# Kernel tuning notes

Measured on AMD Instinct MI355X. Metric: run time of the kernel, lower is better.

The kernel has to match this reference:

```python
import jax, jax.numpy as jnp
import numpy as np


def _gru_step(h, x, Wih, Whh, bih, bhh):
    # PyTorch GRU cell: gates ordered (r, z, n)
    gi = x @ Wih.T + bih
    gh = h @ Whh.T + bhh
    ir, iz, inn = jnp.split(gi, 3, axis=-1)
    hr, hz, hn = jnp.split(gh, 3, axis=-1)
    r = jax.nn.sigmoid(ir + hr)
    u = jax.nn.sigmoid(iz + hz)
    n = jnp.tanh(inn + r * hn)
    return (1.0 - u) * n + u * h


def _forward(mini_batch, eps, W_ih1, W_hh1, b_ih1, b_hh1, W_ih2, W_hh2, b_ih2, b_hh2,
             h1_0, h2_0, Wt1, bt1, Wloc, bloc, Wsc, bsc, We1, be1, We2, be2, We3, be3):
    B = mini_batch.shape[0]
    x_tbf = jnp.swapaxes(mini_batch, 0, 1)      # [T,B,dim_x]
    eps_tbf = jnp.swapaxes(eps, 0, 1)           # [T,B,dim_z]
    h2_init = jnp.broadcast_to(h2_0, (B, h2_0.shape[0]))
    h1_init = jnp.broadcast_to(h1_0, (B, h1_0.shape[0]))

    # gen_RNN_2 over full sequence (all seq_lengths == T, pack/pad is identity)
    def scan2(h, x):
        h = _gru_step(h, x, W_ih2, W_hh2, b_ih2, b_hh2)
        return h, h
    _, h2_seq = jax.lax.scan(scan2, h2_init, x_tbf)              # [T,B,dim_h2]
    # at step t the emitter sees h2_output[t-2] (h2_0 for t==1): shift right by one
    h2_shift = jnp.concatenate([h2_init[None], h2_seq[:-1]], axis=0)

    def step(h1, inp):
        eps_t, h2_t = inp
        # stoch_trans (dz): MLP -> z_loc, z_scale
        hid = jax.nn.relu(h1 @ Wt1.T + bt1)
        z_loc = hid @ Wloc.T + bloc
        z_scale = jax.nn.softplus(hid @ Wsc.T + bsc)
        z_t = z_loc + z_scale * eps_t                            # reparameterized sample
        h1n = _gru_step(h1, z_t, W_ih1, W_hh1, b_ih1, b_hh1)     # gen_RNN_1 one step
        dx_in = jnp.concatenate([h1n, h2_t], axis=-1)            # [B, dim_h1+dim_h2]
        e = jax.nn.relu(dx_in @ We1.T + be1)                     # emitter (dx)
        e = jax.nn.relu(e @ We2.T + be2)
        x_ps = jax.nn.sigmoid(e @ We3.T + be3)                   # Bernoulli probs
        return h1n, x_ps

    _, xps = jax.lax.scan(step, h1_init, (eps_tbf, h2_shift))    # [T,B,dim_x]
    return jnp.swapaxes(xps, 0, 1)                               # [B,T,dim_x]


def setup_inputs() -> dict:
    key = jax.random.key(0)
    B, T = 256, 1000
    DX, DZ, H1, H2, DDX, DDZ = 100, 100, 10, 10, 20, 20
    ks = jax.random.split(key, 24)
    f32 = jnp.float32
    w = lambda k, shape: (jax.random.normal(k, shape, f32) * 0.1)
    inp = {
        "mini_batch": (jax.random.uniform(ks[0], (B, T, DX)) < 0.5).astype(f32),
        "eps": jax.random.normal(ks[1], (B, T, DZ), f32),
        # gen_RNN_1: input dim_z -> hidden dim_h1
        "W_ih1": w(ks[2], (3 * H1, DZ)), "W_hh1": w(ks[3], (3 * H1, H1)),
        "b_ih1": w(ks[4], (3 * H1,)), "b_hh1": w(ks[5], (3 * H1,)),
        # gen_RNN_2: input dim_x -> hidden dim_h2
        "W_ih2": w(ks[6], (3 * H2, DX)), "W_hh2": w(ks[7], (3 * H2, H2)),
        "b_ih2": w(ks[8], (3 * H2,)), "b_hh2": w(ks[9], (3 * H2,)),
        "h1_0": jnp.zeros((H1,), f32), "h2_0": jnp.zeros((H2,), f32),
        # stoch_trans (dz): dim_h1 -> dim_dz -> (dim_z loc, dim_z scale)
        "Wt1": w(ks[10], (DDZ, H1)), "bt1": w(ks[11], (DDZ,)),
        "Wloc": w(ks[12], (DZ, DDZ)), "bloc": w(ks[13], (DZ,)),
        "Wsc": w(ks[14], (DZ, DDZ)), "bsc": w(ks[15], (DZ,)),
        # emitter (dx): (dim_h1+dim_h2) -> dim_dx -> dim_dx -> dim_x, sigmoid
        "We1": w(ks[16], (DDX, H1 + H2)), "be1": w(ks[17], (DDX,)),
        "We2": w(ks[18], (DDX, DDX)), "be2": w(ks[19], (DDX,)),
        "We3": w(ks[20], (DX, DDX)), "be3": w(ks[21], (DX,)),
    }
    return inp


def reference(mini_batch, eps, W_ih1, W_hh1, b_ih1, b_hh1, W_ih2, W_hh2, b_ih2, b_hh2,
              h1_0, h2_0, Wt1, bt1, Wloc, bloc, Wsc, bsc, We1, be1, We2, be2, We3, be3):
    return _forward(mini_batch, eps, W_ih1, W_hh1, b_ih1, b_hh1, W_ih2, W_hh2, b_ih2, b_hh2,
                    h1_0, h2_0, Wt1, bt1, Wloc, bloc, Wsc, bsc, We1, be1, We2, be2, We3, be3)
```

## Files before the change

### kernel.cpp

```cpp
#include <hip/hip_runtime.h>
#include <cstdint>

#define T_LEN 1000
#define NB    256

typedef float v2f __attribute__((ext_vector_type(2)));

__device__ __forceinline__ float rcpf_(float x)     { return __builtin_amdgcn_rcpf(x); }
__device__ __forceinline__ float sigmoidf_(float x) { return rcpf_(1.f + __expf(-x)); }
__device__ __forceinline__ float tanhf_(float x) {
    float e = __expf(2.f * x);
    return 1.f - 2.f * rcpf_(e + 1.f);
}
__device__ __forceinline__ float softplusf_(float x) {
    return fmaxf(x, 0.f) + __logf(1.f + __expf(-fabsf(x)));
}
__device__ __forceinline__ float bcast_(float v, int l) {
    return __uint_as_float(__builtin_amdgcn_readlane(__float_as_uint(v), l));
}
__device__ __forceinline__ v2f pkfma_(v2f a, v2f b, v2f c) {
    v2f d;
    asm("v_pk_fma_f32 %0, %1, %2, %3" : "=v"(d) : "v"(a), "v"(b), "v"(c));
    return d;
}

__global__ __launch_bounds__(256) void gi2_kernel(
    const float* __restrict__ x, const float* __restrict__ W,
    const float* __restrict__ bias, float* __restrict__ out)
{
    __shared__ float xsT[100 * 67];

    const int tid = threadIdx.x;
    const int64_t base = (int64_t)blockIdx.x * (64 * 100);
    const float4* gx = (const float4*)(x + base);

#pragma unroll
    for (int it = 0; it < 7; ++it) {
        int i = tid + it * 256;
        if (i < 1600) {
            int r  = i / 25;
            int k4 = i - r * 25;
            float4 v = gx[i];
            xsT[(4 * k4 + 0) * 67 + r] = v.x;
            xsT[(4 * k4 + 1) * 67 + r] = v.y;
            xsT[(4 * k4 + 2) * 67 + r] = v.z;
            xsT[(4 * k4 + 3) * 67 + r] = v.w;
        }
    }
    __syncthreads();

    const int lane = tid & 63;
    const int wv   = __builtin_amdgcn_readfirstlane(tid >> 6);
    const int j0   = wv * 8;

    float acc[8];
#pragma unroll
    for (int jj = 0; jj < 8; ++jj) acc[jj] = 0.f;

    for (int k = 0; k < 100; ++k) {
        float xv = xsT[k * 67 + lane];
#pragma unroll
        for (int jj = 0; jj < 8; ++jj) {
            int j = j0 + jj; j = j > 29 ? 29 : j;
            acc[jj] = fmaf(xv, W[j * 100 + k], acc[jj]);
        }
    }
    float* orow = out + base + (int64_t)lane * 100;
#pragma unroll
    for (int jj = 0; jj < 8; ++jj) {
        int j = j0 + jj;
        if (j < 30) orow[j] = acc[jj] + bias[j];
    }
}

__global__ __launch_bounds__(128) void scan_kernel(
    const float* __restrict__ eps,
    const float* __restrict__ W_ih1, const float* __restrict__ W_hh1,
    const float* __restrict__ b_ih1, const float* __restrict__ b_hh1,
    const float* __restrict__ W_hh2, const float* __restrict__ b_hh2,
    const float* __restrict__ h1_0,  const float* __restrict__ h2_0,
    const float* __restrict__ Wt1,   const float* __restrict__ bt1,
    const float* __restrict__ Wloc,  const float* __restrict__ bloc,
    const float* __restrict__ Wsc,   const float* __restrict__ bsc,
    const float* __restrict__ We1,   const float* __restrict__ be1,
    const float* __restrict__ We2,   const float* __restrict__ be2,
    const float* __restrict__ We3,   const float* __restrict__ be3,
    float* out)
{
    __shared__ __align__(16) float ss[104];
    __shared__ __align__(16) float sh1ring[2][12];

    const int lane = threadIdx.x & 63;
    const int64_t rowbase = (int64_t)blockIdx.x * T_LEN * 100;
    const int wave = __builtin_amdgcn_readfirstlane((int)(threadIdx.x >> 6));

    if (wave == 0) {
        const int j   = lane & 31;
        const int jc  = j < 30 ? j : 29;
        const int h   = lane >> 5;
        const int lt  = lane < 20 ? lane : 19;
        const int k50 = lane < 50 ? lane : 49;

        float wt1r[10], whh1r[10], Cr[20];
        v2f wsc2[20], wbig2[26];
#pragma unroll
        for (int k = 0; k < 10; ++k) {
            wt1r[k]  = Wt1[lt * 10 + k];
            whh1r[k] = W_hh1[jc * 10 + k];
        }
        float bt1r  = bt1[lt];
        float bhh1r = b_hh1[jc];
        float br1   = b_ih1[jc];
#pragma unroll
        for (int l = 0; l < 20; ++l) {
            wsc2[l].x = Wsc[(2 * k50)     * 20 + l];
            wsc2[l].y = Wsc[(2 * k50 + 1) * 20 + l];
        }
        float bscx = bsc[2 * k50], bscy = bsc[2 * k50 + 1];
#pragma unroll
        for (int c = 0; c < 13; ++c) {
#pragma unroll
            for (int d = 0; d < 2; ++d) {
                int i0 = 4 * c + 2 * d;
                v2f w; w.x = 0.f; w.y = 0.f;
                if (i0     < 50) w.x = W_ih1[jc * 100 + 50 * h + i0];
                if (i0 + 1 < 50) w.y = W_ih1[jc * 100 + 50 * h + i0 + 1];
                wbig2[2 * c + d] = w;
            }
        }

        float dr = 0.f;
#pragma unroll
        for (int l = 0; l < 20; ++l) Cr[l] = 0.f;
        for (int kk = 0; kk < 100; ++kk) {
            float w = W_ih1[jc * 100 + kk];
            dr = fmaf(w, bloc[kk], dr);
#pragma unroll
            for (int l = 0; l < 20; ++l) Cr[l] = fmaf(w, Wloc[kk * 20 + l], Cr[l]);
        }

        if (lane < 2) { ss[50 + lane] = 0.f; ss[102 + lane] = 0.f; }

        float h1keep = h1_0[lane < 10 ? lane : 0];
        float sh1_[10];
#pragma unroll
        for (int k = 0; k < 10; ++k) sh1_[k] = h1_0[k];

        const float* erow = eps + rowbase;
        const int sidx = 2 * k50 + (k50 >= 25 ? 2 : 0);
        v2f ecur = *(const v2f*)(erow + 2 * k50);
        v2f enxt = *(const v2f*)(erow + 100 + 2 * k50);

#pragma unroll 1
        for (int t = 0; t <= T_LEN; ++t) {
            if (t < T_LEN) {
                v2f efut; efut.x = 0.f; efut.y = 0.f;
                if (t + 2 < T_LEN)
                    efut = *(const v2f*)(erow + (int64_t)(t + 2) * 100 + 2 * k50);

                float ha = bt1r, hb = 0.f, ga = bhh1r, gb = 0.f;
#pragma unroll
                for (int k = 0; k < 5; ++k) {
                    ha = fmaf(wt1r[2 * k],      sh1_[2 * k],     ha);
                    hb = fmaf(wt1r[2 * k + 1],  sh1_[2 * k + 1], hb);
                    ga = fmaf(whh1r[2 * k],     sh1_[2 * k],     ga);
                    gb = fmaf(whh1r[2 * k + 1], sh1_[2 * k + 1], gb);
                }
                float hidv = fmaxf(ha + hb, 0.f);
                float gh1v = ga + gb;

                float sgh[20];
#pragma unroll
                for (int l = 0; l < 20; ++l) sgh[l] = bcast_(hidv, l);

                float sA0 = bscx, sA1 = 0.f, sB0 = bscy, sB1 = 0.f, q0 = dr, q1 = 0.f;
#pragma unroll
                for (int l = 0; l < 10; ++l) {
                    sA0 = fmaf(wsc2[2 * l].x,     sgh[2 * l],     sA0);
                    sA1 = fmaf(wsc2[2 * l + 1].x, sgh[2 * l + 1], sA1);
                    sB0 = fmaf(wsc2[2 * l].y,     sgh[2 * l],     sB0);
                    sB1 = fmaf(wsc2[2 * l + 1].y, sgh[2 * l + 1], sB1);
                    q0  = fmaf(Cr[2 * l],         sgh[2 * l],     q0);
                    q1  = fmaf(Cr[2 * l + 1],     sgh[2 * l + 1], q1);
                }
                float gq = q0 + q1;
                float zx = softplusf_(sA0 + sA1) * ecur.x;
                float zy = softplusf_(sB0 + sB1) * ecur.y;
                if (lane < 50) {
                    v2f zp; zp.x = zx; zp.y = zy;
                    *(v2f*)(&ss[sidx]) = zp;
                }
                ecur = enxt; enxt = efut;
                __builtin_amdgcn_wave_barrier();

                const float4* sp4 = (const float4*)(&ss[52 * h]);
                v2f a0; a0.x = 0.f; a0.y = 0.f;
                v2f a1 = a0;
#pragma unroll
                for (int c = 0; c < 13; ++c) {
                    float4 v = sp4[c];
                    v2f vlo; vlo.x = v.x; vlo.y = v.y;
                    v2f vhi; vhi.x = v.z; vhi.y = v.w;
                    a0 = pkfma_(wbig2[2 * c],     vlo, a0);
                    a1 = pkfma_(wbig2[2 * c + 1], vhi, a1);
                }
                float p = (a0.x + a0.y) + (a1.x + a1.y);
                float gi1v = p + __shfl_xor(p, 32) + br1 + gq;
                float av   = gi1v + gh1v;
                float a10  = __shfl(av,   lane + 10);
                float gin  = __shfl(gi1v, lane + 20);
                float ghn  = __shfl(gh1v, lane + 20);
                if (lane < 10) {
                    float r = sigmoidf_(av);
                    float u = sigmoidf_(a10);
                    float n = tanhf_(fmaf(r, ghn, gin));
                    h1keep = fmaf(u, h1keep - n, n);
                    sh1ring[t & 1][lane] = h1keep;
                }
#pragma unroll
                for (int k = 0; k < 10; ++k) sh1_[k] = bcast_(h1keep, k);
            }
            __syncthreads();
        }
    } else {
        const int lt20 = lane < 20 ? lane : 19;
        const int l30  = lane < 30 ? lane : 29;
        const int ls   = lane < 50 ? lane : 49;

        float whh2r[10];
#pragma unroll
        for (int k = 0; k < 10; ++k) whh2r[k] = W_hh2[l30 * 10 + k];
        float bhh2r = b_hh2[l30];

        float we1r[20], we2r[20], we3A[20], we3B[20];
#pragma unroll
        for (int k = 0; k < 20; ++k) {
            we1r[k] = We1[lt20 * 20 + k];
            we2r[k] = We2[lt20 * 20 + k];
            we3A[k] = We3[ls * 20 + k];
            we3B[k] = We3[(ls + 50) * 20 + k];
        }
        float be1r = be1[lt20], be2r = be2[lt20];
        float be3A = be3[ls],   be3B = be3[ls + 50];

        float h2keep = h2_0[lane < 10 ? lane : 0];
        float g2c[10], g2p[10];
#pragma unroll
        for (int k = 0; k < 10; ++k) { g2c[k] = h2_0[k]; g2p[k] = h2_0[k]; }

        float gcur = out[rowbase + l30];
        float gnxt = out[rowbase + 100 + l30];

#pragma unroll 1
        for (int t = 0; t <= T_LEN; ++t) {
            float gfut = 0.f;
            if (t + 2 < T_LEN)
                gfut = out[rowbase + (int64_t)(t + 2) * 100 + l30];

            float4 d0 = make_float4(0.f, 0.f, 0.f, 0.f);
            float4 d1 = d0; float d8 = 0.f, d9 = 0.f;
            if (t >= 1) {
                const int s1 = (t - 1) & 1;
                d0 = *(const float4*)(&sh1ring[s1][0]);
                d1 = *(const float4*)(&sh1ring[s1][4]);
                d8 = sh1ring[s1][8]; d9 = sh1ring[s1][9];
            }

            const bool upd = (t < T_LEN);
            if (upd) {
                float ga = bhh2r, gb = 0.f;
#pragma unroll
                for (int k = 0; k < 5; ++k) {
                    ga = fmaf(whh2r[2 * k],     g2c[2 * k],     ga);
                    gb = fmaf(whh2r[2 * k + 1], g2c[2 * k + 1], gb);
                }
                float gh2v = ga + gb;
                float gi2v = gcur;
                gcur = gnxt; gnxt = gfut;
                float a2  = gi2v + gh2v;
                float a10 = __shfl(a2,   lane + 10);
                float gin = __shfl(gi2v, lane + 20);
                float ghn = __shfl(gh2v, lane + 20);
                if (lane < 10) {
                    float r = sigmoidf_(a2);
                    float u = sigmoidf_(a10);
                    float n = tanhf_(fmaf(r, ghn, gin));
                    h2keep = fmaf(u, h2keep - n, n);
                }
            }

            if (t >= 1) {
                float ea = be1r, eb = 0.f;
                ea = fmaf(we1r[0], d0.x, ea); eb = fmaf(we1r[1], d0.y, eb);
                ea = fmaf(we1r[2], d0.z, ea); eb = fmaf(we1r[3], d0.w, eb);
                ea = fmaf(we1r[4], d1.x, ea); eb = fmaf(we1r[5], d1.y, eb);
                ea = fmaf(we1r[6], d1.z, ea); eb = fmaf(we1r[7], d1.w, eb);
                ea = fmaf(we1r[8], d8,   ea); eb = fmaf(we1r[9], d9,   eb);
#pragma unroll
                for (int k = 0; k < 5; ++k) {
                    ea = fmaf(we1r[10 + 2 * k],     g2p[2 * k],     ea);
                    eb = fmaf(we1r[10 + 2 * k + 1], g2p[2 * k + 1], eb);
                }
                float e1v = fmaxf(ea + eb, 0.f);

                float se1v[20];
#pragma unroll
                for (int l = 0; l < 20; ++l) se1v[l] = bcast_(e1v, l);

                float fa = be2r, fb = 0.f;
#pragma unroll
                for (int k = 0; k < 10; ++k) {
                    fa = fmaf(we2r[2 * k],     se1v[2 * k],     fa);
                    fb = fmaf(we2r[2 * k + 1], se1v[2 * k + 1], fb);
                }
                float e2v = fmaxf(fa + fb, 0.f);

                float se2v[20];
#pragma unroll
                for (int l = 0; l < 20; ++l) se2v[l] = bcast_(e2v, l);

                float xa0 = be3A, xa1 = 0.f, xb0 = be3B, xb1 = 0.f;
#pragma unroll
                for (int l = 0; l < 10; ++l) {
                    xa0 = fmaf(we3A[2 * l],     se2v[2 * l],     xa0);
                    xa1 = fmaf(we3A[2 * l + 1], se2v[2 * l + 1], xa1);
                    xb0 = fmaf(we3B[2 * l],     se2v[2 * l],     xb0);
                    xb1 = fmaf(we3B[2 * l + 1], se2v[2 * l + 1], xb1);
                }
                float xA = sigmoidf_(xa0 + xa1);
                float xB = sigmoidf_(xb0 + xb1);
                if (lane < 50) {
                    int64_t ro = rowbase + (int64_t)(t - 1) * 100;
                    out[ro + lane]      = xA;
                    out[ro + lane + 50] = xB;
                }
            }

            if (upd) {
#pragma unroll
                for (int k = 0; k < 10; ++k) g2p[k] = g2c[k];
#pragma unroll
                for (int k = 0; k < 10; ++k) g2c[k] = bcast_(h2keep, k);
            }
            __syncthreads();
        }
    }
}

extern "C" void kernel_launch(void* const* d_in, const int* in_sizes, int n_in,
                              void* d_out, int out_size, void* d_ws, size_t ws_size,
                              hipStream_t stream) {
    const float* mini_batch = (const float*)d_in[0];
    const float* eps        = (const float*)d_in[1];
    const float* W_ih1      = (const float*)d_in[2];
    const float* W_hh1      = (const float*)d_in[3];
    const float* b_ih1      = (const float*)d_in[4];
    const float* b_hh1      = (const float*)d_in[5];
    const float* W_ih2      = (const float*)d_in[6];
    const float* W_hh2      = (const float*)d_in[7];
    const float* b_ih2      = (const float*)d_in[8];
    const float* b_hh2      = (const float*)d_in[9];
    const float* h1_0       = (const float*)d_in[10];
    const float* h2_0       = (const float*)d_in[11];
    const float* Wt1        = (const float*)d_in[12];
    const float* bt1        = (const float*)d_in[13];
    const float* Wloc       = (const float*)d_in[14];
    const float* bloc       = (const float*)d_in[15];
    const float* Wsc        = (const float*)d_in[16];
    const float* bsc        = (const float*)d_in[17];
    const float* We1        = (const float*)d_in[18];
    const float* be1        = (const float*)d_in[19];
    const float* We2        = (const float*)d_in[20];
    const float* be2        = (const float*)d_in[21];
    const float* We3        = (const float*)d_in[22];
    const float* be3        = (const float*)d_in[23];
    float* out = (float*)d_out;

    gi2_kernel<<<(NB * T_LEN) / 64, 256, 0, stream>>>(mini_batch, W_ih2, b_ih2, out);

    scan_kernel<<<NB, 128, 0, stream>>>(eps, W_ih1, W_hh1, b_ih1, b_hh1, W_hh2, b_hh2,
                                        h1_0, h2_0, Wt1, bt1, Wloc, bloc, Wsc, bsc,
                                        We1, be1, We2, be2, We3, be3, out);
}
```

Before: 845.3 us.

## Replace __syncthreads with lgkm-only barrier and drop packed FMA path

```diff
diff --git a/kernel.cpp b/kernel.cpp
--- a/kernel.cpp
+++ b/kernel.cpp
@@ -3,8 +3,6 @@
 
 #define T_LEN 1000
 #define NB    256
-
-typedef float v2f __attribute__((ext_vector_type(2)));
 
 __device__ __forceinline__ float rcpf_(float x)     { return __builtin_amdgcn_rcpf(x); }
 __device__ __forceinline__ float sigmoidf_(float x) { return rcpf_(1.f + __expf(-x)); }
@@ -18,11 +16,8 @@
 __device__ __forceinline__ float bcast_(float v, int l) {
     return __uint_as_float(__builtin_amdgcn_readlane(__float_as_uint(v), l));
 }
-__device__ __forceinline__ v2f pkfma_(v2f a, v2f b, v2f c) {
-    v2f d;
-    asm("v_pk_fma_f32 %0, %1, %2, %3" : "=v"(d) : "v"(a), "v"(b), "v"(c));
-    return d;
-}
+
+#define BARRIER_SYNC() asm volatile("s_waitcnt lgkmcnt(0)\n\ts_barrier" ::: "memory")
 
 __global__ __launch_bounds__(256) void gi2_kernel(
     const float* __restrict__ x, const float* __restrict__ W,
@@ -87,7 +82,7 @@
     const float* __restrict__ We3,   const float* __restrict__ be3,
     float* out)
 {
-    __shared__ __align__(16) float ss[104];
+    __shared__ __align__(16) float ss2[2][52];
     __shared__ __align__(16) float sh1ring[2][12];
 
     const int lane = threadIdx.x & 63;
@@ -95,14 +90,13 @@
     const int wave = __builtin_amdgcn_readfirstlane((int)(threadIdx.x >> 6));
 
     if (wave == 0) {
-        const int j   = lane & 31;
-        const int jc  = j < 30 ? j : 29;
-        const int h   = lane >> 5;
-        const int lt  = lane < 20 ? lane : 19;
-        const int k50 = lane < 50 ? lane : 49;
-
-        float wt1r[10], whh1r[10], Cr[20];
-        v2f wsc2[20], wbig2[26];
+        const int j  = lane & 31;
+        const int jc = j < 30 ? j : 29;
+        const int h  = lane >> 5;
+        const int lt = lane < 20 ? lane : 19;
+        const int ls = lane < 50 ? lane : 49;
+
+        float wt1r[10], whh1r[10], wscA[20], wscB[20], wbig[52], Cr[20];
 #pragma unroll
         for (int k = 0; k < 10; ++k) {
             wt1r[k]  = Wt1[lt * 10 + k];
@@ -113,21 +107,13 @@
         float br1   = b_ih1[jc];
 #pragma unroll
         for (int l = 0; l < 20; ++l) {
-            wsc2[l].x = Wsc[(2 * k50)     * 20 + l];
-            wsc2[l].y = Wsc[(2 * k50 + 1) * 20 + l];
-        }
-        float bscx = bsc[2 * k50], bscy = bsc[2 * k50 + 1];
-#pragma unroll
-        for (int c = 0; c < 13; ++c) {
-#pragma unroll
-            for (int d = 0; d < 2; ++d) {
-                int i0 = 4 * c + 2 * d;
-                v2f w; w.x = 0.f; w.y = 0.f;
-                if (i0     < 50) w.x = W_ih1[jc * 100 + 50 * h + i0];
-                if (i0 + 1 < 50) w.y = W_ih1[jc * 100 + 50 * h + i0 + 1];
-                wbig2[2 * c + d] = w;
-            }
-        }
+            wscA[l] = Wsc[ls * 20 + l];
+            wscB[l] = Wsc[(ls + 50) * 20 + l];
+        }
+        float bscA = bsc[ls], bscB = bsc[ls + 50];
+#pragma unroll
+        for (int i = 0; i < 50; ++i) wbig[i] = W_ih1[jc * 100 + h * 50 + i];
+        wbig[50] = 0.f; wbig[51] = 0.f;
 
         float dr = 0.f;
 #pragma unroll
@@ -139,7 +125,7 @@
             for (int l = 0; l < 20; ++l) Cr[l] = fmaf(w, Wloc[kk * 20 + l], Cr[l]);
         }
 
-        if (lane < 2) { ss[50 + lane] = 0.f; ss[102 + lane] = 0.f; }
+        if (lane < 2) { ss2[0][50 + lane] = 0.f; ss2[1][50 + lane] = 0.f; }
 
         float h1keep = h1_0[lane < 10 ? lane : 0];
         float sh1_[10];
@@ -147,16 +133,15 @@
         for (int k = 0; k < 10; ++k) sh1_[k] = h1_0[k];
 
         const float* erow = eps + rowbase;
-        const int sidx = 2 * k50 + (k50 >= 25 ? 2 : 0);
-        v2f ecur = *(const v2f*)(erow + 2 * k50);
-        v2f enxt = *(const v2f*)(erow + 100 + 2 * k50);
+        float eA0 = erow[ls],        eB0 = erow[ls + 50];
+        float eA1 = erow[100 + ls],  eB1 = erow[100 + ls + 50];
 
 #pragma unroll 1
         for (int t = 0; t <= T_LEN; ++t) {
             if (t < T_LEN) {
-                v2f efut; efut.x = 0.f; efut.y = 0.f;
-                if (t + 2 < T_LEN)
-                    efut = *(const v2f*)(erow + (int64_t)(t + 2) * 100 + 2 * k50);
+                const int tp = t + 2 < T_LEN ? t + 2 : T_LEN - 1;
+                float eAf = erow[(int64_t)tp * 100 + ls];
+                float eBf = erow[(int64_t)tp * 100 + ls + 50];
 
                 float ha = bt1r, hb = 0.f, ga = bhh1r, gb = 0.f;
 #pragma unroll
@@ -173,38 +158,36 @@
 #pragma unroll
                 for (int l = 0; l < 20; ++l) sgh[l] = bcast_(hidv, l);
 
-                float sA0 = bscx, sA1 = 0.f, sB0 = bscy, sB1 = 0.f, q0 = dr, q1 = 0.f;
+                float sA0 = bscA, sA1 = 0.f, sB0 = bscB, sB1 = 0.f, q0 = dr, q1 = 0.f;
 #pragma unroll
                 for (int l = 0; l < 10; ++l) {
-                    sA0 = fmaf(wsc2[2 * l].x,     sgh[2 * l],     sA0);
-                    sA1 = fmaf(wsc2[2 * l + 1].x, sgh[2 * l + 1], sA1);
-                    sB0 = fmaf(wsc2[2 * l].y,     sgh[2 * l],     sB0);
-                    sB1 = fmaf(wsc2[2 * l + 1].y, sgh[2 * l + 1], sB1);
-                    q0  = fmaf(Cr[2 * l],         sgh[2 * l],     q0);
-                    q1  = fmaf(Cr[2 * l + 1],     sgh[2 * l + 1], q1);
+                    sA0 = fmaf(wscA[2 * l],     sgh[2 * l],     sA0);
+                    sA1 = fmaf(wscA[2 * l + 1], sgh[2 * l + 1], sA1);
+                    sB0 = fmaf(wscB[2 * l],     sgh[2 * l],     sB0);
+                    sB1 = fmaf(wscB[2 * l + 1], sgh[2 * l + 1], sB1);
+                    q0  = fmaf(Cr[2 * l],       sgh[2 * l],     q0);
+                    q1  = fmaf(Cr[2 * l + 1],   sgh[2 * l + 1], q1);
                 }
                 float gq = q0 + q1;
-                float zx = softplusf_(sA0 + sA1) * ecur.x;
-                float zy = softplusf_(sB0 + sB1) * ecur.y;
-                if (lane < 50) {
-                    v2f zp; zp.x = zx; zp.y = zy;
-                    *(v2f*)(&ss[sidx]) = zp;
-                }
-                ecur = enxt; enxt = efut;
+                float zA = softplusf_(sA0 + sA1) * eA0;
+                float zB = softplusf_(sB0 + sB1) * eB0;
+                if (lane < 50) { ss2[0][lane] = zA; ss2[1][lane] = zB; }
+
+                eA0 = eA1; eB0 = eB1; eA1 = eAf; eB1 = eBf;
+
                 __builtin_amdgcn_wave_barrier();
 
-                const float4* sp4 = (const float4*)(&ss[52 * h]);
-                v2f a0; a0.x = 0.f; a0.y = 0.f;
-                v2f a1 = a0;
+                const float4* sp4 = (const float4*)(&ss2[h][0]);
+                float p0 = 0.f, p1 = 0.f, p2 = 0.f, p3 = 0.f;
 #pragma unroll
                 for (int c = 0; c < 13; ++c) {
                     float4 v = sp4[c];
-                    v2f vlo; vlo.x = v.x; vlo.y = v.y;
-                    v2f vhi; vhi.x = v.z; vhi.y = v.w;
-                    a0 = pkfma_(wbig2[2 * c],     vlo, a0);
-                    a1 = pkfma_(wbig2[2 * c + 1], vhi, a1);
-                }
-                float p = (a0.x + a0.y) + (a1.x + a1.y);
+                    p0 = fmaf(wbig[4 * c + 0], v.x, p0);
+                    p1 = fmaf(wbig[4 * c + 1], v.y, p1);
+                    p2 = fmaf(wbig[4 * c + 2], v.z, p2);
+                    p3 = fmaf(wbig[4 * c + 3], v.w, p3);
+                }
+                float p = (p0 + p1) + (p2 + p3);
                 float gi1v = p + __shfl_xor(p, 32) + br1 + gq;
                 float av   = gi1v + gh1v;
                 float a10  = __shfl(av,   lane + 10);
@@ -220,7 +203,7 @@
 #pragma unroll
                 for (int k = 0; k < 10; ++k) sh1_[k] = bcast_(h1keep, k);
             }
-            __syncthreads();
+            BARRIER_SYNC();
         }
     } else {
         const int lt20 = lane < 20 ? lane : 19;
@@ -253,9 +236,8 @@
 
 #pragma unroll 1
         for (int t = 0; t <= T_LEN; ++t) {
-            float gfut = 0.f;
-            if (t + 2 < T_LEN)
-                gfut = out[rowbase + (int64_t)(t + 2) * 100 + l30];
+            const int tp = t + 2 < T_LEN ? t + 2 : T_LEN - 1;
+            float gfut = out[rowbase + (int64_t)tp * 100 + l30];
 
             float4 d0 = make_float4(0.f, 0.f, 0.f, 0.f);
             float4 d1 = d0; float d8 = 0.f, d9 = 0.f;
@@ -342,7 +324,7 @@
 #pragma unroll
                 for (int k = 0; k < 10; ++k) g2c[k] = bcast_(h2keep, k);
             }
-            __syncthreads();
+            BARRIER_SYNC();
         }
     }
 }
```

New measurement: 834.0 us. Within noise of the previous version (-1.3%).
